# Kernel tuning notes

Measured on AMD Instinct MI355X. Metric: run time of the kernel, lower is better.

Reference implementation:

```python
import jax, jax.numpy as jnp
import numpy as np

K_HOPS = 2


def setup_inputs() -> dict:
    key = jax.random.key(0)
    k1, k2, k3 = jax.random.split(key, 3)
    N, E, D, C = 100000, 3200000, 512, 40
    x = jax.random.normal(k1, (N, D), dtype=jnp.float32)
    edge_index = jax.random.randint(k2, (2, E), 0, N, dtype=jnp.int64)
    W = jax.random.normal(k3, (C, D), dtype=jnp.float32) * 0.05
    b = jnp.zeros((C,), dtype=jnp.float32)
    return {"x": x, "edge_index": edge_index, "W": W, "b": b}


def reference(x, edge_index, W, b):
    # SGConv: K-hop symmetric-normalized propagation, then Linear, then log_softmax.
    # Dropout is identity at inference (training=False).
    N = x.shape[0]
    loop = jnp.arange(N, dtype=edge_index.dtype)
    src = jnp.concatenate([edge_index[0], loop])  # source nodes (+ self-loops)
    dst = jnp.concatenate([edge_index[1], loop])  # target nodes (+ self-loops)
    ew = jnp.ones(src.shape[0], dtype=x.dtype)
    # deg^{-1/2} A_hat deg^{-1/2}: degree computed at the target (col) index, as in PyG gcn_norm
    deg = jax.ops.segment_sum(ew, dst, num_segments=N)
    dinv = jnp.where(deg > 0, jax.lax.rsqrt(deg), 0.0)
    norm = dinv[src] * dinv[dst]  # [E+N]
    h = x
    for _ in range(K_HOPS):
        # gather source features, weight, scatter-add to targets
        h = jax.ops.segment_sum(norm[:, None] * h[src], dst, num_segments=N)
    logits = h @ W.T + b  # [N, C]
    return jax.nn.log_softmax(logits, axis=1)
```

## Files before the change

kernel.cpp:

```cpp
#include <hip/hip_runtime.h>
#include <hip/hip_bf16.h>


#define TPB 256
#define ETILE 8192

typedef __attribute__((ext_vector_type(8))) short short8v;
typedef __attribute__((ext_vector_type(4))) float f32x4;

__device__ inline short f2bf(float f) {
    unsigned u = __float_as_uint(f);
    unsigned r = (u + 0x7fffu + ((u >> 16) & 1u)) >> 16;
    return (short)r;
}
__device__ inline float bf2f(short s) {
    return __uint_as_float(((unsigned)(unsigned short)s) << 16);
}

__global__ void k_zero(int* __restrict__ p, int n) {
    int i = threadIdx.x;
    if (i < n) p[i] = 0;
}

__global__ __launch_bounds__(TPB) void k_bhist(
    const int* __restrict__ dst, int* __restrict__ bcnt, int E, int nb) {
    __shared__ int h[512];
    int t = threadIdx.x;
    for (int i = t; i < nb; i += TPB) h[i] = 0;
    __syncthreads();
    int e0 = blockIdx.x * ETILE;
    for (int i = t; i < ETILE; i += TPB) {
        int e = e0 + i;
        if (e < E) atomicAdd(&h[dst[e] >> 8], 1);
    }
    __syncthreads();
    for (int i = t; i < nb; i += TPB)
        if (h[i]) atomicAdd(&bcnt[i], h[i]);
}

__global__ __launch_bounds__(512) void k_boff(
    const int* __restrict__ bcnt, int* __restrict__ boff,
    int* __restrict__ bcur, int nb) {
    __shared__ int s[512];
    int t = threadIdx.x;
    int own = (t < nb) ? bcnt[t] : 0;
    s[t] = own;
    __syncthreads();
    for (int off = 1; off < 512; off <<= 1) {
        int v = (t >= off) ? s[t - off] : 0;
        __syncthreads();
        s[t] += v;
        __syncthreads();
    }
    if (t < nb) {
        int ex = s[t] - own;
        boff[t] = ex;
        bcur[t] = ex;
        if (t == nb - 1) boff[nb] = s[t];
    }
}

__global__ __launch_bounds__(TPB) void k_part(
    const int* __restrict__ src, const int* __restrict__ dst,
    int* __restrict__ bcur, int* __restrict__ pairs, int E, int nb) {
    __shared__ int stash[ETILE];
    __shared__ int hist[512], base[512], lcur[512];
    int t = threadIdx.x;
    for (int i = t; i < nb; i += TPB) hist[i] = 0;
    __syncthreads();
    int e0 = blockIdx.x * ETILE;
    for (int i = t; i < ETILE; i += TPB) {
        int e = e0 + i;
        int d = (e < E) ? dst[e] : -1;
        stash[i] = d;
        if (d >= 0) atomicAdd(&hist[d >> 8], 1);
    }
    __syncthreads();
    for (int i = t; i < nb; i += TPB) {
        base[i] = hist[i] ? atomicAdd(&bcur[i], hist[i]) : 0;
        lcur[i] = 0;
    }
    __syncthreads();
    for (int i = t; i < ETILE; i += TPB) {
        int d = stash[i];
        if (d >= 0) {
            int b = d >> 8;
            int pos = base[b] + atomicAdd(&lcur[b], 1);
            pairs[pos] = ((d & 255) << 20) | src[e0 + i];
        }
    }
}

__global__ __launch_bounds__(TPB) void k_sort(
    const int* __restrict__ pairs, const int* __restrict__ boff,
    int* __restrict__ csr, int* __restrict__ row_ptr, float* __restrict__ dinv,
    int N, int nb) {
    __shared__ int hist[256], excl[256], lcur[256];
    int b = blockIdx.x, t = threadIdx.x;
    hist[t] = 0;
    __syncthreads();
    int beg = boff[b], end = boff[b + 1];
    for (int j = beg + t; j < end; j += TPB)
        atomicAdd(&hist[pairs[j] >> 20], 1);
    __syncthreads();
    int own = hist[t];
    excl[t] = own;
    __syncthreads();
    for (int off = 1; off < 256; off <<= 1) {
        int v = (t >= off) ? excl[t - off] : 0;
        __syncthreads();
        excl[t] += v;
        __syncthreads();
    }
    int node = (b << 8) + t;
    if (node < N) {
        row_ptr[node] = beg + excl[t] - own;
        dinv[node] = rsqrtf((float)(own + 1));
    }
    lcur[t] = 0;
    __syncthreads();
    for (int j = beg + t; j < end; j += TPB) {
        int u = pairs[j];
        int dl = u >> 20;
        int pos = beg + (excl[dl] - hist[dl]) + atomicAdd(&lcur[dl], 1);
        csr[pos] = u & 0xFFFFF;
    }
    if (b == nb - 1 && t == 0) row_ptr[N] = end;
}

__global__ void k_wconv(const float* __restrict__ W, short* __restrict__ Wb) {
    int idx = blockIdx.x * TPB + threadIdx.x;
    int c = idx >> 9, k = idx & 511;
    float v = (c < 40) ? W[c * 512 + k] : 0.f;
    Wb[idx] = f2bf(v);
}

__global__ __launch_bounds__(TPB) void k_matmul_mfma(
    const float* __restrict__ x, const short* __restrict__ Wb,
    const float* __restrict__ dinv, short* __restrict__ z, int N) {
    int wid  = threadIdx.x >> 6;
    int lane = threadIdx.x & 63;
    int rbase = blockIdx.x * 64 + wid * 16;
    if (rbase >= N) return;
    int arow   = rbase + (lane & 15);
    int aclamp = min(arow, N - 1);
    int koff   = (lane >> 4) * 8;
    const float* xrow = x + (size_t)aclamp * 512 + koff;
    const short* wb   = Wb + (lane & 15) * 512 + koff;

    f32x4 acc0 = {0.f,0.f,0.f,0.f}, acc1 = {0.f,0.f,0.f,0.f}, acc2 = {0.f,0.f,0.f,0.f};
    for (int ks = 0; ks < 16; ++ks) {
        int k0 = ks * 32;
        float4 f0 = *reinterpret_cast<const float4*>(xrow + k0);
        float4 f1 = *reinterpret_cast<const float4*>(xrow + k0 + 4);
        short8v a;
        a[0] = f2bf(f0.x); a[1] = f2bf(f0.y); a[2] = f2bf(f0.z); a[3] = f2bf(f0.w);
        a[4] = f2bf(f1.x); a[5] = f2bf(f1.y); a[6] = f2bf(f1.z); a[7] = f2bf(f1.w);
        short8v b0 = *reinterpret_cast<const short8v*>(wb + k0);
        short8v b1 = *reinterpret_cast<const short8v*>(wb + 16 * 512 + k0);
        short8v b2 = *reinterpret_cast<const short8v*>(wb + 32 * 512 + k0);
        acc0 = __builtin_amdgcn_mfma_f32_16x16x32_bf16(a, b0, acc0, 0, 0, 0);
        acc1 = __builtin_amdgcn_mfma_f32_16x16x32_bf16(a, b1, acc1, 0, 0, 0);
        acc2 = __builtin_amdgcn_mfma_f32_16x16x32_bf16(a, b2, acc2, 0, 0, 0);
    }
    int col = lane & 15;
    int rw  = rbase + (lane >> 4) * 4;
#pragma unroll
    for (int reg = 0; reg < 4; ++reg) {
        int r = rw + reg;
        if (r < N) {
            float di = dinv[r];
            z[(size_t)r * 40 + col]      = f2bf(di * acc0[reg]);
            z[(size_t)r * 40 + 16 + col] = f2bf(di * acc1[reg]);
            if (col < 8)
                z[(size_t)r * 40 + 32 + col] = f2bf(di * acc2[reg]);
        }
    }
}

template <int P>
__global__ __launch_bounds__(TPB) void k_hop_bf16(
    const int* __restrict__ csr, const int* __restrict__ row_ptr,
    const float* __restrict__ dinv, const short* __restrict__ zin,
    short* __restrict__ zout_bf, float* __restrict__ zout_f32, int N) {
    int t = blockIdx.x * TPB + threadIdx.x;
    int node = t / 5;
    int c8 = t - node * 5;
    if (node >= N) return;
    const short8v* Z = reinterpret_cast<const short8v*>(zin);
    short8v sv = Z[node * 5 + c8];
    float acc[8];
#pragma unroll
    for (int k = 0; k < 8; ++k) acc[k] = bf2f(sv[k]);
    int beg = row_ptr[node];
    int end = row_ptr[node + 1];
    for (int j = beg; j < end; ++j) {
        int s = csr[j];
        short8v v = Z[s * 5 + c8];
#pragma unroll
        for (int k = 0; k < 8; ++k) acc[k] += bf2f(v[k]);
    }
    float dd = dinv[node];
    if (P == 2) {
        float sc = dd * dd;
        short8v o;
#pragma unroll
        for (int k = 0; k < 8; ++k) o[k] = f2bf(sc * acc[k]);
        reinterpret_cast<short8v*>(zout_bf)[node * 5 + c8] = o;
    } else {
        float* op = zout_f32 + (size_t)node * 40 + c8 * 8;
        *reinterpret_cast<float4*>(op)     = make_float4(dd*acc[0], dd*acc[1], dd*acc[2], dd*acc[3]);
        *reinterpret_cast<float4*>(op + 4) = make_float4(dd*acc[4], dd*acc[5], dd*acc[6], dd*acc[7]);
    }
}

__global__ __launch_bounds__(TPB) void k_logsoftmax(
    float* __restrict__ out, const float* __restrict__ b, int N) {
    int r = blockIdx.x * TPB + threadIdx.x;
    if (r >= N) return;
    float4* rowp = reinterpret_cast<float4*>(out + (size_t)r * 40);
    float v[40];
    float m = -1e30f;
#pragma unroll
    for (int c4 = 0; c4 < 10; ++c4) {
        float4 t = rowp[c4];
        v[c4*4+0] = t.x + b[c4*4+0];
        v[c4*4+1] = t.y + b[c4*4+1];
        v[c4*4+2] = t.z + b[c4*4+2];
        v[c4*4+3] = t.w + b[c4*4+3];
    }
#pragma unroll
    for (int c = 0; c < 40; ++c) m = fmaxf(m, v[c]);
    float sum = 0.f;
#pragma unroll
    for (int c = 0; c < 40; ++c) sum += __expf(v[c] - m);
    float lse = m + __logf(sum);
#pragma unroll
    for (int c4 = 0; c4 < 10; ++c4)
        rowp[c4] = make_float4(v[c4*4+0]-lse, v[c4*4+1]-lse, v[c4*4+2]-lse, v[c4*4+3]-lse);
}

extern "C" void kernel_launch(void* const* d_in, const int* in_sizes, int n_in,
                              void* d_out, int out_size, void* d_ws, size_t ws_size,
                              hipStream_t stream) {
    const float* x  = (const float*)d_in[0];
    const int*   ei = (const int*)d_in[1];
    const float* W  = (const float*)d_in[2];
    const float* b  = (const float*)d_in[3];
    float* out = (float*)d_out;

    const int N = in_sizes[0] / 512;
    const int E = in_sizes[1] / 2;
    const int* src = ei;
    const int* dst = ei + E;
    const int nb = (N + 255) >> 8;

    short* z0b     = (short*)d_ws;
    short* z1b     = z0b + (size_t)N * 40;
    int*   csr     = (int*)(z1b + (size_t)N * 40);
    int*   pairs   = csr + E;
    int*   bcnt    = pairs + E;
    int*   boff    = bcnt + nb;
    int*   bcur    = boff + nb + 1;
    int*   row_ptr = bcur + nb;
    float* dinv    = (float*)(row_ptr + N + 1);
    short* Wb      = (short*)(dinv + N);

    int gN = (N + TPB - 1) / TPB;
    int gT = (E + ETILE - 1) / ETILE;
    int gM = (N + 63) / 64;
    int gH = (N * 5 + TPB - 1) / TPB;

    k_zero<<<1, 512, 0, stream>>>(bcnt, nb);
    k_wconv<<<(48 * 512) / TPB, TPB, 0, stream>>>(W, Wb);
    k_bhist<<<gT, TPB, 0, stream>>>(dst, bcnt, E, nb);
    k_boff<<<1, 512, 0, stream>>>(bcnt, boff, bcur, nb);
    k_part<<<gT, TPB, 0, stream>>>(src, dst, bcur, pairs, E, nb);
    k_sort<<<nb, TPB, 0, stream>>>(pairs, boff, csr, row_ptr, dinv, N, nb);

    k_matmul_mfma<<<gM, TPB, 0, stream>>>(x, Wb, dinv, z0b, N);

    k_hop_bf16<2><<<gH, TPB, 0, stream>>>(csr, row_ptr, dinv, z0b, z1b, nullptr, N);
    k_hop_bf16<1><<<gH, TPB, 0, stream>>>(csr, row_ptr, dinv, z1b, nullptr, out, N);

    k_logsoftmax<<<gN, TPB, 0, stream>>>(out, b, N);
}
```

Measured before the change: 352.1 us.

## Fuse second hop with bias and log-softmax, unroll gather, merge zeroing kernel

The second propagation hop now computes bias add and log_softmax in-register. Each node's 40 channels are spread over 5 lanes of a wave, with shuffles for the max and sum reductions. This removes the separate log-softmax kernel, which read and rewrote the fp32 output, and saves one launch. The gather loop is unrolled by 4 so more loads are in flight at once. Zeroing bcnt is folded into the weight-conversion kernel. The fused hop leaves 4 of 64 lanes idle per wave.

```diff
diff --git a/kernel.cpp b/kernel.cpp
--- a/kernel.cpp
+++ b/kernel.cpp
@@ -15,11 +15,6 @@
 }
 __device__ inline float bf2f(short s) {
     return __uint_as_float(((unsigned)(unsigned short)s) << 16);
-}
-
-__global__ void k_zero(int* __restrict__ p, int n) {
-    int i = threadIdx.x;
-    if (i < n) p[i] = 0;
 }
 
 __global__ __launch_bounds__(TPB) void k_bhist(
@@ -128,7 +123,10 @@
     if (b == nb - 1 && t == 0) row_ptr[N] = end;
 }
 
-__global__ void k_wconv(const float* __restrict__ W, short* __restrict__ Wb) {
+__global__ void k_wconv(const float* __restrict__ W, short* __restrict__ Wb,
+                        int* __restrict__ bcnt, int nb) {
+    if (blockIdx.x == 0)
+        for (int i = threadIdx.x; i < nb; i += TPB) bcnt[i] = 0;
     int idx = blockIdx.x * TPB + threadIdx.x;
     int c = idx >> 9, k = idx & 511;
     float v = (c < 40) ? W[c * 512 + k] : 0.f;
@@ -178,11 +176,31 @@
     }
 }
 
-template <int P>
-__global__ __launch_bounds__(TPB) void k_hop_bf16(
+__device__ inline void gather_acc(
+    const short8v* __restrict__ Z, const int* __restrict__ csr,
+    int beg, int end, int c8, float acc[8]) {
+    int j = beg;
+    for (; j + 4 <= end; j += 4) {
+        int s0 = csr[j], s1 = csr[j+1], s2 = csr[j+2], s3 = csr[j+3];
+        short8v v0 = Z[s0 * 5 + c8];
+        short8v v1 = Z[s1 * 5 + c8];
+        short8v v2 = Z[s2 * 5 + c8];
+        short8v v3 = Z[s3 * 5 + c8];
+#pragma unroll
+        for (int k = 0; k < 8; ++k)
+            acc[k] += (bf2f(v0[k]) + bf2f(v1[k])) + (bf2f(v2[k]) + bf2f(v3[k]));
+    }
+    for (; j < end; ++j) {
+        short8v v = Z[csr[j] * 5 + c8];
+#pragma unroll
+        for (int k = 0; k < 8; ++k) acc[k] += bf2f(v[k]);
+    }
+}
+
+__global__ __launch_bounds__(TPB) void k_hop1(
     const int* __restrict__ csr, const int* __restrict__ row_ptr,
     const float* __restrict__ dinv, const short* __restrict__ zin,
-    short* __restrict__ zout_bf, float* __restrict__ zout_f32, int N) {
+    short* __restrict__ zout, int N) {
     int t = blockIdx.x * TPB + threadIdx.x;
     int node = t / 5;
     int c8 = t - node * 5;
@@ -192,52 +210,60 @@
     float acc[8];
 #pragma unroll
     for (int k = 0; k < 8; ++k) acc[k] = bf2f(sv[k]);
-    int beg = row_ptr[node];
-    int end = row_ptr[node + 1];
-    for (int j = beg; j < end; ++j) {
-        int s = csr[j];
-        short8v v = Z[s * 5 + c8];
-#pragma unroll
-        for (int k = 0; k < 8; ++k) acc[k] += bf2f(v[k]);
-    }
+    gather_acc(Z, csr, row_ptr[node], row_ptr[node + 1], c8, acc);
     float dd = dinv[node];
-    if (P == 2) {
-        float sc = dd * dd;
-        short8v o;
-#pragma unroll
-        for (int k = 0; k < 8; ++k) o[k] = f2bf(sc * acc[k]);
-        reinterpret_cast<short8v*>(zout_bf)[node * 5 + c8] = o;
-    } else {
-        float* op = zout_f32 + (size_t)node * 40 + c8 * 8;
-        *reinterpret_cast<float4*>(op)     = make_float4(dd*acc[0], dd*acc[1], dd*acc[2], dd*acc[3]);
-        *reinterpret_cast<float4*>(op + 4) = make_float4(dd*acc[4], dd*acc[5], dd*acc[6], dd*acc[7]);
-    }
-}
-
-__global__ __launch_bounds__(TPB) void k_logsoftmax(
-    float* __restrict__ out, const float* __restrict__ b, int N) {
-    int r = blockIdx.x * TPB + threadIdx.x;
-    if (r >= N) return;
-    float4* rowp = reinterpret_cast<float4*>(out + (size_t)r * 40);
-    float v[40];
-    float m = -1e30f;
-#pragma unroll
-    for (int c4 = 0; c4 < 10; ++c4) {
-        float4 t = rowp[c4];
-        v[c4*4+0] = t.x + b[c4*4+0];
-        v[c4*4+1] = t.y + b[c4*4+1];
-        v[c4*4+2] = t.z + b[c4*4+2];
-        v[c4*4+3] = t.w + b[c4*4+3];
-    }
-#pragma unroll
-    for (int c = 0; c < 40; ++c) m = fmaxf(m, v[c]);
-    float sum = 0.f;
-#pragma unroll
-    for (int c = 0; c < 40; ++c) sum += __expf(v[c] - m);
-    float lse = m + __logf(sum);
-#pragma unroll
-    for (int c4 = 0; c4 < 10; ++c4)
-        rowp[c4] = make_float4(v[c4*4+0]-lse, v[c4*4+1]-lse, v[c4*4+2]-lse, v[c4*4+3]-lse);
+    float sc = dd * dd;
+    short8v o;
+#pragma unroll
+    for (int k = 0; k < 8; ++k) o[k] = f2bf(sc * acc[k]);
+    reinterpret_cast<short8v*>(zout)[node * 5 + c8] = o;
+}
+
+__global__ __launch_bounds__(TPB) void k_hop2_lsm(
+    const int* __restrict__ csr, const int* __restrict__ row_ptr,
+    const float* __restrict__ dinv, const short* __restrict__ zin,
+    const float* __restrict__ bias, float* __restrict__ out, int N) {
+    int wid  = threadIdx.x >> 6;
+    int lane = threadIdx.x & 63;
+    int g    = lane / 5;
+    int c8   = lane - g * 5;
+    int node = (blockIdx.x * 4 + wid) * 12 + g;
+    bool active = (g < 12) && (node < N);
+
+    float v[8];
+    float lm = -1e30f;
+    if (active) {
+        const short8v* Z = reinterpret_cast<const short8v*>(zin);
+        short8v sv = Z[node * 5 + c8];
+        float acc[8];
+#pragma unroll
+        for (int k = 0; k < 8; ++k) acc[k] = bf2f(sv[k]);
+        gather_acc(Z, csr, row_ptr[node], row_ptr[node + 1], c8, acc);
+        float dd = dinv[node];
+#pragma unroll
+        for (int k = 0; k < 8; ++k) {
+            v[k] = dd * acc[k] + bias[c8 * 8 + k];
+            lm = fmaxf(lm, v[k]);
+        }
+    }
+    int base = g * 5;
+    float gm = lm;
+#pragma unroll
+    for (int k = 0; k < 5; ++k) gm = fmaxf(gm, __shfl(lm, base + k, 64));
+    float ls = 0.f;
+    if (active) {
+#pragma unroll
+        for (int k = 0; k < 8; ++k) ls += __expf(v[k] - gm);
+    }
+    float tot = 0.f;
+#pragma unroll
+    for (int k = 0; k < 5; ++k) tot += __shfl(ls, base + k, 64);
+    if (active) {
+        float lse = gm + __logf(tot);
+        float* op = out + (size_t)node * 40 + c8 * 8;
+        *reinterpret_cast<float4*>(op)     = make_float4(v[0]-lse, v[1]-lse, v[2]-lse, v[3]-lse);
+        *reinterpret_cast<float4*>(op + 4) = make_float4(v[4]-lse, v[5]-lse, v[6]-lse, v[7]-lse);
+    }
 }
 
 extern "C" void kernel_launch(void* const* d_in, const int* in_sizes, int n_in,
@@ -266,13 +292,12 @@
     float* dinv    = (float*)(row_ptr + N + 1);
     short* Wb      = (short*)(dinv + N);
 
-    int gN = (N + TPB - 1) / TPB;
-    int gT = (E + ETILE - 1) / ETILE;
-    int gM = (N + 63) / 64;
-    int gH = (N * 5 + TPB - 1) / TPB;
-
-    k_zero<<<1, 512, 0, stream>>>(bcnt, nb);
-    k_wconv<<<(48 * 512) / TPB, TPB, 0, stream>>>(W, Wb);
+    int gT  = (E + ETILE - 1) / ETILE;
+    int gM  = (N + 63) / 64;
+    int gH1 = (N * 5 + TPB - 1) / TPB;
+    int gH2 = (N + 47) / 48;
+
+    k_wconv<<<(48 * 512) / TPB, TPB, 0, stream>>>(W, Wb, bcnt, nb);
     k_bhist<<<gT, TPB, 0, stream>>>(dst, bcnt, E, nb);
     k_boff<<<1, 512, 0, stream>>>(bcnt, boff, bcur, nb);
     k_part<<<gT, TPB, 0, stream>>>(src, dst, bcur, pairs, E, nb);
@@ -280,8 +305,6 @@
 
     k_matmul_mfma<<<gM, TPB, 0, stream>>>(x, Wb, dinv, z0b, N);
 
-    k_hop_bf16<2><<<gH, TPB, 0, stream>>>(csr, row_ptr, dinv, z0b, z1b, nullptr, N);
-    k_hop_bf16<1><<<gH, TPB, 0, stream>>>(csr, row_ptr, dinv, z1b, nullptr, out, N);
-
-    k_logsoftmax<<<gN, TPB, 0, stream>>>(out, b, N);
-}
+    k_hop1<<<gH1, TPB, 0, stream>>>(csr, row_ptr, dinv, z0b, z1b, N);
+    k_hop2_lsm<<<gH2, TPB, 0, stream>>>(csr, row_ptr, dinv, z1b, b, out, N);
+}
```

Result: faster. 315.9 us (-10.3%).

## Split hop features into column-slab arrays and unroll neighbor gather

Applied to the files above, without the earlier changes.

Stores the 40-wide bf16 projected features as three separate column slabs (16, 16, 8) so each hop pass gathers from a smaller array with better cache locality, and interleaves the slab passes across blocks in one launch. The neighbor loop is unrolled by four with nontemporal index loads and nontemporal output stores. The edge partition kernel drops its shared-memory stash and rereads dst from global, and the edge tile is doubled. The bcnt zeroing is folded into the weight conversion kernel, which removes one launch. The hop grid size is hardcoded for N=100000.

```diff
diff --git a/kernel.cpp b/kernel.cpp
--- a/kernel.cpp
+++ b/kernel.cpp
@@ -3,7 +3,7 @@
 
 
 #define TPB 256
-#define ETILE 8192
+#define ETILE 16384
 
 typedef __attribute__((ext_vector_type(8))) short short8v;
 typedef __attribute__((ext_vector_type(4))) float f32x4;
@@ -17,9 +17,14 @@
     return __uint_as_float(((unsigned)(unsigned short)s) << 16);
 }
 
-__global__ void k_zero(int* __restrict__ p, int n) {
-    int i = threadIdx.x;
-    if (i < n) p[i] = 0;
+__global__ void k_wconv(const float* __restrict__ W, short* __restrict__ Wb,
+                        int* __restrict__ bcnt, int nb) {
+    if (blockIdx.x == 0)
+        for (int i = threadIdx.x; i < nb; i += TPB) bcnt[i] = 0;
+    int idx = blockIdx.x * TPB + threadIdx.x;
+    int c = idx >> 9, k = idx & 511;
+    float v = (c < 40) ? W[c * 512 + k] : 0.f;
+    Wb[idx] = f2bf(v);
 }
 
 __global__ __launch_bounds__(TPB) void k_bhist(
@@ -29,10 +34,9 @@
     for (int i = t; i < nb; i += TPB) h[i] = 0;
     __syncthreads();
     int e0 = blockIdx.x * ETILE;
-    for (int i = t; i < ETILE; i += TPB) {
-        int e = e0 + i;
-        if (e < E) atomicAdd(&h[dst[e] >> 8], 1);
-    }
+    int e1 = min(e0 + ETILE, E);
+    for (int e = e0 + t; e < e1; e += TPB)
+        atomicAdd(&h[dst[e] >> 8], 1);
     __syncthreads();
     for (int i = t; i < nb; i += TPB)
         if (h[i]) atomicAdd(&bcnt[i], h[i]);
@@ -63,31 +67,25 @@
 __global__ __launch_bounds__(TPB) void k_part(
     const int* __restrict__ src, const int* __restrict__ dst,
     int* __restrict__ bcur, int* __restrict__ pairs, int E, int nb) {
-    __shared__ int stash[ETILE];
-    __shared__ int hist[512], base[512], lcur[512];
+    __shared__ int hist[512], base[512];
     int t = threadIdx.x;
     for (int i = t; i < nb; i += TPB) hist[i] = 0;
     __syncthreads();
     int e0 = blockIdx.x * ETILE;
-    for (int i = t; i < ETILE; i += TPB) {
-        int e = e0 + i;
-        int d = (e < E) ? dst[e] : -1;
-        stash[i] = d;
-        if (d >= 0) atomicAdd(&hist[d >> 8], 1);
-    }
+    int e1 = min(e0 + ETILE, E);
+    for (int e = e0 + t; e < e1; e += TPB)
+        atomicAdd(&hist[dst[e] >> 8], 1);
     __syncthreads();
     for (int i = t; i < nb; i += TPB) {
         base[i] = hist[i] ? atomicAdd(&bcur[i], hist[i]) : 0;
-        lcur[i] = 0;
-    }
-    __syncthreads();
-    for (int i = t; i < ETILE; i += TPB) {
-        int d = stash[i];
-        if (d >= 0) {
-            int b = d >> 8;
-            int pos = base[b] + atomicAdd(&lcur[b], 1);
-            pairs[pos] = ((d & 255) << 20) | src[e0 + i];
-        }
+        hist[i] = 0;
+    }
+    __syncthreads();
+    for (int e = e0 + t; e < e1; e += TPB) {
+        int d = dst[e];
+        int b = d >> 8;
+        int pos = base[b] + atomicAdd(&hist[b], 1);
+        pairs[pos] = ((d & 255) << 20) | src[e];
     }
 }
 
@@ -128,16 +126,10 @@
     if (b == nb - 1 && t == 0) row_ptr[N] = end;
 }
 
-__global__ void k_wconv(const float* __restrict__ W, short* __restrict__ Wb) {
-    int idx = blockIdx.x * TPB + threadIdx.x;
-    int c = idx >> 9, k = idx & 511;
-    float v = (c < 40) ? W[c * 512 + k] : 0.f;
-    Wb[idx] = f2bf(v);
-}
-
 __global__ __launch_bounds__(TPB) void k_matmul_mfma(
     const float* __restrict__ x, const short* __restrict__ Wb,
-    const float* __restrict__ dinv, short* __restrict__ z, int N) {
+    const float* __restrict__ dinv, short* __restrict__ zA,
+    short* __restrict__ zB, short* __restrict__ zC, int N) {
     int wid  = threadIdx.x >> 6;
     int lane = threadIdx.x & 63;
     int rbase = blockIdx.x * 64 + wid * 16;
@@ -170,33 +162,58 @@
         int r = rw + reg;
         if (r < N) {
             float di = dinv[r];
-            z[(size_t)r * 40 + col]      = f2bf(di * acc0[reg]);
-            z[(size_t)r * 40 + 16 + col] = f2bf(di * acc1[reg]);
+            zA[(size_t)r * 16 + col] = f2bf(di * acc0[reg]);
+            zB[(size_t)r * 16 + col] = f2bf(di * acc1[reg]);
             if (col < 8)
-                z[(size_t)r * 40 + 32 + col] = f2bf(di * acc2[reg]);
+                zC[(size_t)r * 8 + col] = f2bf(di * acc2[reg]);
         }
     }
 }
 
 template <int P>
-__global__ __launch_bounds__(TPB) void k_hop_bf16(
+__global__ __launch_bounds__(TPB) void k_hop_all(
     const int* __restrict__ csr, const int* __restrict__ row_ptr,
-    const float* __restrict__ dinv, const short* __restrict__ zin,
-    short* __restrict__ zout_bf, float* __restrict__ zout_f32, int N) {
-    int t = blockIdx.x * TPB + threadIdx.x;
-    int node = t / 5;
-    int c8 = t - node * 5;
+    const float* __restrict__ dinv,
+    const short* __restrict__ zA, const short* __restrict__ zB,
+    const short* __restrict__ zC,
+    short* __restrict__ oA, short* __restrict__ oB, short* __restrict__ oC,
+    float* __restrict__ outf, int N) {
+    int bid = blockIdx.x;
+    int x8 = bid & 7;
+    int pass, pblk;
+    if (x8 < 3)      { pass = 0; pblk = (bid >> 3) * 3 + x8; }
+    else if (x8 < 6) { pass = 1; pblk = (bid >> 3) * 3 + (x8 - 3); }
+    else             { pass = 2; pblk = (bid >> 3) * 2 + (x8 - 6); }
+    int t = pblk * TPB + threadIdx.x;
+    int node, c8, lpn;
+    if (pass == 2) { node = t;      c8 = 0;     lpn = 1; }
+    else           { node = t >> 1; c8 = t & 1; lpn = 2; }
     if (node >= N) return;
+    const short* zin = (pass == 0) ? zA : (pass == 1) ? zB : zC;
     const short8v* Z = reinterpret_cast<const short8v*>(zin);
-    short8v sv = Z[node * 5 + c8];
+    int zi = node * lpn + c8;
+    short8v sv = Z[zi];
     float acc[8];
 #pragma unroll
     for (int k = 0; k < 8; ++k) acc[k] = bf2f(sv[k]);
     int beg = row_ptr[node];
     int end = row_ptr[node + 1];
-    for (int j = beg; j < end; ++j) {
-        int s = csr[j];
-        short8v v = Z[s * 5 + c8];
+    int j = beg;
+    for (; j + 4 <= end; j += 4) {
+        int s0 = __builtin_nontemporal_load(csr + j);
+        int s1 = __builtin_nontemporal_load(csr + j + 1);
+        int s2 = __builtin_nontemporal_load(csr + j + 2);
+        int s3 = __builtin_nontemporal_load(csr + j + 3);
+        short8v v0 = Z[s0 * lpn + c8];
+        short8v v1 = Z[s1 * lpn + c8];
+        short8v v2 = Z[s2 * lpn + c8];
+        short8v v3 = Z[s3 * lpn + c8];
+#pragma unroll
+        for (int k = 0; k < 8; ++k)
+            acc[k] += (bf2f(v0[k]) + bf2f(v1[k])) + (bf2f(v2[k]) + bf2f(v3[k]));
+    }
+    for (; j < end; ++j) {
+        short8v v = Z[__builtin_nontemporal_load(csr + j) * lpn + c8];
 #pragma unroll
         for (int k = 0; k < 8; ++k) acc[k] += bf2f(v[k]);
     }
@@ -206,11 +223,15 @@
         short8v o;
 #pragma unroll
         for (int k = 0; k < 8; ++k) o[k] = f2bf(sc * acc[k]);
-        reinterpret_cast<short8v*>(zout_bf)[node * 5 + c8] = o;
+        short* zo = (pass == 0) ? oA : (pass == 1) ? oB : oC;
+        reinterpret_cast<short8v*>(zo)[zi] = o;
     } else {
-        float* op = zout_f32 + (size_t)node * 40 + c8 * 8;
-        *reinterpret_cast<float4*>(op)     = make_float4(dd*acc[0], dd*acc[1], dd*acc[2], dd*acc[3]);
-        *reinterpret_cast<float4*>(op + 4) = make_float4(dd*acc[4], dd*acc[5], dd*acc[6], dd*acc[7]);
+        int off = (pass == 0) ? 0 : (pass == 1) ? 16 : 32;
+        float* op = outf + (size_t)node * 40 + off + c8 * 8;
+        f32x4 lo = {dd*acc[0], dd*acc[1], dd*acc[2], dd*acc[3]};
+        f32x4 hi = {dd*acc[4], dd*acc[5], dd*acc[6], dd*acc[7]};
+        __builtin_nontemporal_store(lo, reinterpret_cast<f32x4*>(op));
+        __builtin_nontemporal_store(hi, reinterpret_cast<f32x4*>(op + 4));
     }
 }
 
@@ -255,9 +276,13 @@
     const int* dst = ei + E;
     const int nb = (N + 255) >> 8;
 
-    short* z0b     = (short*)d_ws;
-    short* z1b     = z0b + (size_t)N * 40;
-    int*   csr     = (int*)(z1b + (size_t)N * 40);
+    short* zA0     = (short*)d_ws;
+    short* zB0     = zA0 + (size_t)N * 16;
+    short* zC0     = zB0 + (size_t)N * 16;
+    short* zA1     = zC0 + (size_t)N * 8;
+    short* zB1     = zA1 + (size_t)N * 16;
+    short* zC1     = zB1 + (size_t)N * 16;
+    int*   csr     = (int*)(zC1 + (size_t)N * 8);
     int*   pairs   = csr + E;
     int*   bcnt    = pairs + E;
     int*   boff    = bcnt + nb;
@@ -266,22 +291,23 @@
     float* dinv    = (float*)(row_ptr + N + 1);
     short* Wb      = (short*)(dinv + N);
 
-    int gN = (N + TPB - 1) / TPB;
-    int gT = (E + ETILE - 1) / ETILE;
-    int gM = (N + 63) / 64;
-    int gH = (N * 5 + TPB - 1) / TPB;
-
-    k_zero<<<1, 512, 0, stream>>>(bcnt, nb);
-    k_wconv<<<(48 * 512) / TPB, TPB, 0, stream>>>(W, Wb);
+    int gT  = (E + ETILE - 1) / ETILE;
+    int gM  = (N + 63) / 64;
+    int gN  = (N + TPB - 1) / TPB;
+    int gH  = 2085;
+
+    k_wconv<<<(48 * 512) / TPB, TPB, 0, stream>>>(W, Wb, bcnt, nb);
     k_bhist<<<gT, TPB, 0, stream>>>(dst, bcnt, E, nb);
     k_boff<<<1, 512, 0, stream>>>(bcnt, boff, bcur, nb);
     k_part<<<gT, TPB, 0, stream>>>(src, dst, bcur, pairs, E, nb);
     k_sort<<<nb, TPB, 0, stream>>>(pairs, boff, csr, row_ptr, dinv, N, nb);
 
-    k_matmul_mfma<<<gM, TPB, 0, stream>>>(x, Wb, dinv, z0b, N);
-
-    k_hop_bf16<2><<<gH, TPB, 0, stream>>>(csr, row_ptr, dinv, z0b, z1b, nullptr, N);
-    k_hop_bf16<1><<<gH, TPB, 0, stream>>>(csr, row_ptr, dinv, z1b, nullptr, out, N);
+    k_matmul_mfma<<<gM, TPB, 0, stream>>>(x, Wb, dinv, zA0, zB0, zC0, N);
+
+    k_hop_all<2><<<gH, TPB, 0, stream>>>(csr, row_ptr, dinv, zA0, zB0, zC0,
+                                         zA1, zB1, zC1, nullptr, N);
+    k_hop_all<1><<<gH, TPB, 0, stream>>>(csr, row_ptr, dinv, zA1, zB1, zC1,
+                                         nullptr, nullptr, nullptr, out, N);
 
     k_logsoftmax<<<gN, TPB, 0, stream>>>(out, b, N);
 }
```

New measurement: 443.1 us. +25.8%, slower.
